# Kernel optimization log

Measured on AMD Instinct MI355X. Metric: run time of the kernel, lower is better.

## Reference

```python
import jax, jax.numpy as jnp
import numpy as np

B, C, R, E, H = 32, 64, 63, 256, 4
D = E // H  # head dim = 64


def setup_inputs() -> dict:
    key = jax.random.key(0)
    ks = jax.random.split(key, 8)
    s = 0.02
    return {
        "x": jax.random.normal(ks[0], (B, C, R, E), jnp.float32),
        "real_cols": jax.random.randint(ks[1], (B,), 0, C),
        "cls_token": jax.random.normal(ks[2], (E,), jnp.float32),
        "w_in": (jax.random.normal(ks[3], (3 * E, E), jnp.float32) * s),
        "b_in": jnp.zeros((3 * E,), jnp.float32),
        "w_out": (jax.random.normal(ks[4], (E, E), jnp.float32) * s),
        "b_out": jnp.zeros((E,), jnp.float32),
        "ln_g": jnp.ones((E,), jnp.float32),
        "ln_b": jnp.zeros((E,), jnp.float32),
        "w1": (jax.random.normal(ks[5], (E, E), jnp.float32) * s),
        "b1": jnp.zeros((E,), jnp.float32),
        "w2": (jax.random.normal(ks[6], (E, E), jnp.float32) * s),
        "b2": jnp.zeros((E,), jnp.float32),
    }


def reference(x, real_cols, cls_token, w_in, b_in, w_out, b_out, ln_g, ln_b, w1, b1, w2, b2):
    # x: (B, C, R, E); one fused batched MHA+LN+FFN over all (B, C) columns.
    Bq, Cq, Rq, Eq = x.shape
    S = Rq + 1
    cls = jnp.broadcast_to(cls_token, (Bq, Cq, 1, Eq))
    seq = jnp.concatenate([cls, x], axis=2)  # (B,C,S,E)

    # torch MultiheadAttention in-projection: x @ W^T + b, packed q|k|v
    qkv = seq @ w_in.T + b_in  # (B,C,S,3E)
    q, k, v = jnp.split(qkv, 3, axis=-1)
    q = q.reshape(Bq, Cq, S, H, D)
    k = k.reshape(Bq, Cq, S, H, D)
    v = v.reshape(Bq, Cq, S, H, D)

    scale = 1.0 / jnp.sqrt(jnp.asarray(D, x.dtype))
    scores = jnp.einsum('bcqhd,bckhd->bchqk', q, k) * scale  # (B,C,H,S,S)
    attn = jax.nn.softmax(scores, axis=-1)
    ctx = jnp.einsum('bchqk,bckhd->bcqhd', attn, v).reshape(Bq, Cq, S, Eq)
    attn_out = ctx @ w_out.T + b_out  # (B,C,S,E)

    # LayerNorm (biased variance, eps=1e-5 as in torch)
    mu = attn_out.mean(axis=-1, keepdims=True)
    var = ((attn_out - mu) ** 2).mean(axis=-1, keepdims=True)
    ln = (attn_out - mu) / jnp.sqrt(var + 1e-5) * ln_g + ln_b

    ffn = jax.nn.relu(ln @ w1.T + b1) @ w2.T + b2
    out = ln + ffn  # (B,C,S,E)

    rep = out[:, :, 0, :]  # rep_mode == 'cls'

    # columns >= real_cols[b] are zero-padded, matching the original loop
    mask = jnp.arange(Cq)[None, :] < real_cols[:, None]
    return jnp.where(mask[..., None], rep, jnp.zeros((), x.dtype))
```

## Files before the change

### kernel.cpp

```cpp
#include <hip/hip_runtime.h>
#include <hip/hip_bf16.h>
#include <cstdint>

typedef unsigned short u16;
typedef uint32_t u32;

#define Bq 32
#define Cq 64
#define Rq 63
#define NB 4

__device__ __forceinline__ float bflo(u32 u){ return __uint_as_float(u << 16); }
__device__ __forceinline__ float bfhi(u32 u){ return __uint_as_float(u & 0xffff0000u); }
__device__ __forceinline__ float bf1(u16 u){ return __uint_as_float(((u32)u) << 16); }
__device__ __forceinline__ u16 tobf(float f){ __hip_bfloat16 h = __float2bfloat16(f); return *(u16*)&h; }

__device__ __forceinline__ bool dtype_is_bf16(const void* ln_g){
    return *(const u32*)ln_g == 0x3F803F80u;
}
__device__ __forceinline__ float ldin(const void* p, int i, bool bf){
    return bf ? bf1(((const u16*)p)[i]) : ((const float*)p)[i];
}


__global__ __launch_bounds__(256) void prep_kernel(
    const void* __restrict__ cls, const void* __restrict__ w_in,
    const void* __restrict__ b_in, const void* __restrict__ w_out,
    const void* __restrict__ w1, const void* __restrict__ w2,
    const void* __restrict__ ln_g_flag,
    float* __restrict__ uf, float* __restrict__ sbf,
    u16* __restrict__ wvT, u16* __restrict__ woT,
    u16* __restrict__ w1T, u16* __restrict__ w2T)
{
    const bool bf = dtype_is_bf16(ln_g_flag);
    const int tid = threadIdx.x;
    const int blk = blockIdx.x;
    __shared__ float q0[256];
    __shared__ float clsf[256];

    if (blk < 256) {
        const int e = blk, j = tid;
        const int dsti = ((j >> 3) * 256 + e) * 8 + (j & 7);
        wvT[dsti] = tobf(ldin(w_in, (512 + e) * 256 + j, bf));
        woT[dsti] = tobf(ldin(w_out, e * 256 + j, bf));
        w1T[dsti] = tobf(ldin(w1,    e * 256 + j, bf));
        w2T[dsti] = tobf(ldin(w2,    e * 256 + j, bf));
        return;
    }

    const int h = blk - 256;
    clsf[tid] = ldin(cls, tid, bf);
    __syncthreads();

    {
        float acc = ldin(b_in, tid, bf);
        #pragma unroll 8
        for (int j = 0; j < 256; ++j)
            acc += ldin(w_in, tid * 256 + j, bf) * clsf[j];
        q0[tid] = acc;
    }
    __syncthreads();

    {
        float ua = 0.f;
        #pragma unroll 8
        for (int d = 0; d < 64; ++d)
            ua += q0[h * 64 + d] * ldin(w_in, (256 + h * 64 + d) * 256 + tid, bf);
        uf[h * 256 + tid] = ua * 0.125f;
    }
    if (tid < 64) {
        float p = q0[h * 64 + tid] * ldin(b_in, 256 + h * 64 + tid, bf);
        #pragma unroll
        for (int off = 32; off; off >>= 1) p += __shfl_xor(p, off);
        if (tid == 0) sbf[h] = p * 0.125f;
    }
}

__global__ __launch_bounds__(256) void attn_kernel(
    const void* __restrict__ x, const int* __restrict__ real_cols,
    const void* __restrict__ cls, const void* __restrict__ ln_g,
    const float* __restrict__ uf, const float* __restrict__ sbf,
    u16* __restrict__ sbuf)
{
    const bool bf = dtype_is_bf16(ln_g);
    const int tid = threadIdx.x;
    const int bc = blockIdx.x;
    const int b = bc >> 6, c = bc & 63;
    if (c >= real_cols[b]) return;

    __shared__ __align__(16) u16   lds_seq[64 * 260];
    __shared__ __align__(16) float lds_u[1024];
    __shared__ __align__(16) float lds_a[256];
    __shared__ float lds_sb[4];

    #pragma unroll
    for (int q = 0; q < 4; ++q) lds_u[q * 256 + tid] = uf[q * 256 + tid];
    if (tid < 4) lds_sb[tid] = sbf[tid];

    if (bf) {
        const u16* xr = (const u16*)x + (size_t)bc * (Rq * 256);
        #pragma unroll
        for (int k = 0; k < 8; ++k) {
            int idx = k * 256 + tid;
            if (idx < 2016) {
                uint4 val = *(const uint4*)(xr + idx * 8);
                int tt = (idx >> 5) + 1;
                int col = (idx & 31) * 8;
                uint2* p = (uint2*)&lds_seq[tt * 260 + col];
                p[0] = make_uint2(val.x, val.y);
                p[1] = make_uint2(val.z, val.w);
            }
        }
        if (tid < 32) {
            uint4 val = *(const uint4*)((const u16*)cls + tid * 8);
            uint2* p = (uint2*)&lds_seq[tid * 8];
            p[0] = make_uint2(val.x, val.y);
            p[1] = make_uint2(val.z, val.w);
        }
    } else {
        const float* xr = (const float*)x + (size_t)bc * (Rq * 256);
        #pragma unroll
        for (int k = 0; k < 16; ++k) {
            int idx = k * 256 + tid;
            if (idx < 4032) {
                float4 v = *(const float4*)(xr + idx * 4);
                int tt = (idx >> 6) + 1;
                int col = (idx & 63) * 4;
                u32 lo = ((u32)tobf(v.y) << 16) | tobf(v.x);
                u32 hi = ((u32)tobf(v.w) << 16) | tobf(v.z);
                *(uint2*)&lds_seq[tt * 260 + col] = make_uint2(lo, hi);
            }
        }
        if (tid < 64) {
            float4 v = *(const float4*)((const float*)cls + tid * 4);
            u32 lo = ((u32)tobf(v.y) << 16) | tobf(v.x);
            u32 hi = ((u32)tobf(v.w) << 16) | tobf(v.z);
            *(uint2*)&lds_seq[tid * 4] = make_uint2(lo, hi);
        }
    }
    __syncthreads();

    const int h = tid >> 6, t = tid & 63;
    float sc = lds_sb[h];
    {
        const u16* srow = &lds_seq[t * 260];
        const float* uh = &lds_u[h * 256];
        #pragma unroll 8
        for (int j = 0; j < 256; j += 4) {
            uint2 pv = *(const uint2*)&srow[j];
            float4 uv = *(const float4*)&uh[j];
            sc += bflo(pv.x) * uv.x + bfhi(pv.x) * uv.y
                + bflo(pv.y) * uv.z + bfhi(pv.y) * uv.w;
        }
    }
    float m = sc;
    #pragma unroll
    for (int off = 32; off; off >>= 1) m = fmaxf(m, __shfl_xor(m, off));
    float ev = __expf(sc - m);
    float sum = ev;
    #pragma unroll
    for (int off = 32; off; off >>= 1) sum += __shfl_xor(sum, off);
    lds_a[t * 4 + h] = ev / sum;
    __syncthreads();

    {
        float s0 = 0.f, s1 = 0.f, s2 = 0.f, s3 = 0.f;
        #pragma unroll 4
        for (int tt = 0; tt < 64; ++tt) {
            float v = bf1(lds_seq[tt * 260 + tid]);
            float4 at = *(const float4*)&lds_a[tt * 4];
            s0 += at.x * v; s1 += at.y * v; s2 += at.z * v; s3 += at.w * v;
        }
        u16* sp = sbuf + (size_t)bc * 1024;
        sp[tid]       = tobf(s0);
        sp[256 + tid] = tobf(s1);
        sp[512 + tid] = tobf(s2);
        sp[768 + tid] = tobf(s3);
    }
}

template<int NBv>
__device__ __forceinline__ void dotN(const u16* __restrict__ wp,
                                     const float* __restrict__ vecs, int vstride,
                                     float* __restrict__ acc)
{
    #pragma unroll 2
    for (int j8 = 0; j8 < 32; ++j8) {
        uint4 w = *(const uint4*)(wp + j8 * 2048);
        float w0 = bflo(w.x), w1_ = bfhi(w.x), w2_ = bflo(w.y), w3 = bfhi(w.y);
        float w4 = bflo(w.z), w5 = bfhi(w.z), w6 = bflo(w.w), w7 = bfhi(w.w);
        #pragma unroll
        for (int i = 0; i < NBv; ++i) {
            const float* v = vecs + i * vstride + j8 * 8;
            float4 a = *(const float4*)v;
            float4 bq = *(const float4*)(v + 4);
            acc[i] += w0 * a.x + w1_ * a.y + w2_ * a.z + w3 * a.w
                    + w4 * bq.x + w5 * bq.y + w6 * bq.z + w7 * bq.w;
        }
    }
}

__global__ __launch_bounds__(256) void ffn_kernel(
    const int* __restrict__ real_cols,
    const void* __restrict__ b_in, const void* __restrict__ b_out,
    const void* __restrict__ ln_g, const void* __restrict__ ln_b,
    const void* __restrict__ b1p, const void* __restrict__ b2p,
    const u16* __restrict__ sbuf,
    const u16* __restrict__ wvT, const u16* __restrict__ woT,
    const u16* __restrict__ w1T, const u16* __restrict__ w2T,
    void* __restrict__ out)
{
    const bool bf = dtype_is_bf16(ln_g);
    const int tid = threadIdx.x;
    const int b = blockIdx.x >> 4;
    const int g = blockIdx.x & 15;
    const int c0 = g * NB;
    const int rc = real_cols[b];
    const int e = tid;

    if (c0 >= rc) {
        #pragma unroll
        for (int i = 0; i < NB; ++i) {
            size_t oi = (((size_t)b << 6) + c0 + i) * 256 + e;
            if (bf) ((u16*)out)[oi] = 0; else ((float*)out)[oi] = 0.f;
        }
        return;
    }

    __shared__ __align__(16) float lds_s[NB * 1024];
    __shared__ __align__(16) float lds_ctx[NB * 256];
    __shared__ __align__(16) float lds_ln[NB * 256];
    __shared__ __align__(16) float lds_h1[NB * 256];
    __shared__ float lds_redA[4 * NB];
    __shared__ float lds_redB[4 * NB];

    #pragma unroll
    for (int i = 0; i < NB; ++i) {
        int c = c0 + i;
        if (c < rc) {
            const u32* sp = (const u32*)(sbuf + ((((size_t)b << 6) + c) << 10));
            u32 a0 = sp[tid], a1 = sp[tid + 256];
            lds_s[i * 1024 + 2 * tid]       = bflo(a0);
            lds_s[i * 1024 + 2 * tid + 1]   = bfhi(a0);
            lds_s[i * 1024 + 512 + 2 * tid]     = bflo(a1);
            lds_s[i * 1024 + 512 + 2 * tid + 1] = bfhi(a1);
        } else {
            lds_s[i * 1024 + 2 * tid] = 0.f;   lds_s[i * 1024 + 2 * tid + 1] = 0.f;
            lds_s[i * 1024 + 512 + 2 * tid] = 0.f; lds_s[i * 1024 + 512 + 2 * tid + 1] = 0.f;
        }
    }
    __syncthreads();

    const int h = tid >> 6;

    {
        float acc[NB];
        float bv = ldin(b_in, 512 + e, bf);
        #pragma unroll
        for (int i = 0; i < NB; ++i) acc[i] = bv;
        dotN<NB>(wvT + e * 8, &lds_s[h * 256], 1024, acc);
        #pragma unroll
        for (int i = 0; i < NB; ++i) lds_ctx[i * 256 + e] = acc[i];
    }
    __syncthreads();

    float ao[NB];
    {
        float bo = ldin(b_out, e, bf);
        #pragma unroll
        for (int i = 0; i < NB; ++i) ao[i] = bo;
        dotN<NB>(woT + e * 8, lds_ctx, 256, ao);
    }

    const int lane = tid & 63, wv = tid >> 6;
    float mu[NB];
    {
        float r[NB];
        #pragma unroll
        for (int i = 0; i < NB; ++i) r[i] = ao[i];
        #pragma unroll
        for (int off = 32; off; off >>= 1) {
            #pragma unroll
            for (int i = 0; i < NB; ++i) r[i] += __shfl_xor(r[i], off);
        }
        if (lane == 0) {
            #pragma unroll
            for (int i = 0; i < NB; ++i) lds_redA[wv * NB + i] = r[i];
        }
    }
    __syncthreads();
    #pragma unroll
    for (int i = 0; i < NB; ++i)
        mu[i] = (lds_redA[i] + lds_redA[NB + i] + lds_redA[2 * NB + i] + lds_redA[3 * NB + i]) * (1.f / 256.f);

    float lnv[NB];
    {
        float r[NB];
        #pragma unroll
        for (int i = 0; i < NB; ++i) { float d = ao[i] - mu[i]; r[i] = d * d; }
        #pragma unroll
        for (int off = 32; off; off >>= 1) {
            #pragma unroll
            for (int i = 0; i < NB; ++i) r[i] += __shfl_xor(r[i], off);
        }
        if (lane == 0) {
            #pragma unroll
            for (int i = 0; i < NB; ++i) lds_redB[wv * NB + i] = r[i];
        }
    }
    __syncthreads();
    {
        float gg = ldin(ln_g, e, bf), bb = ldin(ln_b, e, bf);
        #pragma unroll
        for (int i = 0; i < NB; ++i) {
            float var = (lds_redB[i] + lds_redB[NB + i] + lds_redB[2 * NB + i] + lds_redB[3 * NB + i]) * (1.f / 256.f);
            lnv[i] = (ao[i] - mu[i]) * rsqrtf(var + 1e-5f) * gg + bb;
            lds_ln[i * 256 + e] = lnv[i];
        }
    }
    __syncthreads();

    {
        float h1[NB];
        float bv = ldin(b1p, e, bf);
        #pragma unroll
        for (int i = 0; i < NB; ++i) h1[i] = bv;
        dotN<NB>(w1T + e * 8, lds_ln, 256, h1);
        #pragma unroll
        for (int i = 0; i < NB; ++i) lds_h1[i * 256 + e] = fmaxf(h1[i], 0.f);
    }
    __syncthreads();

    {
        float o[NB];
        float bv = ldin(b2p, e, bf);
        #pragma unroll
        for (int i = 0; i < NB; ++i) o[i] = lnv[i] + bv;
        dotN<NB>(w2T + e * 8, lds_h1, 256, o);
        #pragma unroll
        for (int i = 0; i < NB; ++i) {
            int c = c0 + i;
            float val = (c < rc) ? o[i] : 0.f;
            size_t oi = (((size_t)b << 6) + c) * 256 + e;
            if (bf) ((u16*)out)[oi] = tobf(val); else ((float*)out)[oi] = val;
        }
    }
}

extern "C" void kernel_launch(void* const* d_in, const int* in_sizes, int n_in,
                              void* d_out, int out_size, void* d_ws, size_t ws_size,
                              hipStream_t stream) {
    const void* x     = d_in[0];
    const int* rcols  = (const int*)d_in[1];
    const void* cls   = d_in[2];
    const void* w_in  = d_in[3];
    const void* b_in  = d_in[4];
    const void* w_out = d_in[5];
    const void* b_out = d_in[6];
    const void* ln_g  = d_in[7];
    const void* ln_b  = d_in[8];
    const void* w1    = d_in[9];
    const void* b1    = d_in[10];
    const void* w2    = d_in[11];
    const void* b2    = d_in[12];

    char* ws = (char*)d_ws;
    float* uf  = (float*)(ws);
    float* sbf = (float*)(ws + 4096);
    u16* wvT = (u16*)(ws + 4608);
    u16* woT = (u16*)(ws + 4608 + 131072);
    u16* w1T = (u16*)(ws + 4608 + 2 * 131072);
    u16* w2T = (u16*)(ws + 4608 + 3 * 131072);
    u16* sbuf = (u16*)(ws + 528896);

    prep_kernel<<<260, 256, 0, stream>>>(cls, w_in, b_in, w_out, w1, w2, ln_g,
                                         uf, sbf, wvT, woT, w1T, w2T);
    attn_kernel<<<Bq * Cq, 256, 0, stream>>>(x, rcols, cls, ln_g, uf, sbf, sbuf);
    ffn_kernel<<<Bq * (Cq / NB), 256, 0, stream>>>(rcols, b_in, b_out, ln_g, ln_b,
                                                   b1, b2, sbuf,
                                                   wvT, woT, w1T, w2T, d_out);
}
```

Measured before the change: 276.6 us.

## Split FFN reductions across two thread halves and move weight transpose into attention launch

The weight transpose/bf16 conversion blocks move from the prep kernel into extra blocks of the attention launch. This shortens the serial prep step so it no longer delays attention. The FFN kernel now uses 512 threads, with each half computing half of the K-dimension dot products and combining partials through LDS, giving more parallelism per block at the cost of extra syncs. The attention weighted-sum stage uses 128 threads, each handling two adjacent elements with packed 32-bit loads and stores.

Result: slower. 293.4 us (+6.1%).

```diff
diff --git a/kernel.cpp b/kernel.cpp
--- a/kernel.cpp
+++ b/kernel.cpp
@@ -23,32 +23,17 @@
 }
 
 
-__global__ __launch_bounds__(256) void prep_kernel(
+__global__ __launch_bounds__(256) void prep_u_kernel(
     const void* __restrict__ cls, const void* __restrict__ w_in,
-    const void* __restrict__ b_in, const void* __restrict__ w_out,
-    const void* __restrict__ w1, const void* __restrict__ w2,
-    const void* __restrict__ ln_g_flag,
-    float* __restrict__ uf, float* __restrict__ sbf,
-    u16* __restrict__ wvT, u16* __restrict__ woT,
-    u16* __restrict__ w1T, u16* __restrict__ w2T)
+    const void* __restrict__ b_in, const void* __restrict__ ln_g_flag,
+    float* __restrict__ uf, float* __restrict__ sbf)
 {
     const bool bf = dtype_is_bf16(ln_g_flag);
     const int tid = threadIdx.x;
-    const int blk = blockIdx.x;
+    const int h = blockIdx.x;
     __shared__ float q0[256];
     __shared__ float clsf[256];
 
-    if (blk < 256) {
-        const int e = blk, j = tid;
-        const int dsti = ((j >> 3) * 256 + e) * 8 + (j & 7);
-        wvT[dsti] = tobf(ldin(w_in, (512 + e) * 256 + j, bf));
-        woT[dsti] = tobf(ldin(w_out, e * 256 + j, bf));
-        w1T[dsti] = tobf(ldin(w1,    e * 256 + j, bf));
-        w2T[dsti] = tobf(ldin(w2,    e * 256 + j, bf));
-        return;
-    }
-
-    const int h = blk - 256;
     clsf[tid] = ldin(cls, tid, bf);
     __syncthreads();
 
@@ -79,12 +64,27 @@
 __global__ __launch_bounds__(256) void attn_kernel(
     const void* __restrict__ x, const int* __restrict__ real_cols,
     const void* __restrict__ cls, const void* __restrict__ ln_g,
+    const void* __restrict__ w_in, const void* __restrict__ w_out,
+    const void* __restrict__ w1, const void* __restrict__ w2,
     const float* __restrict__ uf, const float* __restrict__ sbf,
+    u16* __restrict__ wvT, u16* __restrict__ woT,
+    u16* __restrict__ w1T, u16* __restrict__ w2T,
     u16* __restrict__ sbuf)
 {
     const bool bf = dtype_is_bf16(ln_g);
     const int tid = threadIdx.x;
     const int bc = blockIdx.x;
+
+    if (bc >= 2048) {
+        const int e2 = bc - 2048, j = tid;
+        const int dsti = ((j >> 3) * 256 + e2) * 8 + (j & 7);
+        wvT[dsti] = tobf(ldin(w_in, (512 + e2) * 256 + j, bf));
+        woT[dsti] = tobf(ldin(w_out, e2 * 256 + j, bf));
+        w1T[dsti] = tobf(ldin(w1,    e2 * 256 + j, bf));
+        w2T[dsti] = tobf(ldin(w2,    e2 * 256 + j, bf));
+        return;
+    }
+
     const int b = bc >> 6, c = bc & 63;
     if (c >= real_cols[b]) return;
 
@@ -163,29 +163,33 @@
     lds_a[t * 4 + h] = ev / sum;
     __syncthreads();
 
-    {
-        float s0 = 0.f, s1 = 0.f, s2 = 0.f, s3 = 0.f;
+    if (tid < 128) {
+        const int j2 = tid;
+        float s00 = 0.f, s01 = 0.f, s02 = 0.f, s03 = 0.f;
+        float s10 = 0.f, s11 = 0.f, s12 = 0.f, s13 = 0.f;
         #pragma unroll 4
         for (int tt = 0; tt < 64; ++tt) {
-            float v = bf1(lds_seq[tt * 260 + tid]);
+            u32 pv = *(const u32*)&lds_seq[tt * 260 + 2 * j2];
+            float vlo = bflo(pv), vhi = bfhi(pv);
             float4 at = *(const float4*)&lds_a[tt * 4];
-            s0 += at.x * v; s1 += at.y * v; s2 += at.z * v; s3 += at.w * v;
-        }
-        u16* sp = sbuf + (size_t)bc * 1024;
-        sp[tid]       = tobf(s0);
-        sp[256 + tid] = tobf(s1);
-        sp[512 + tid] = tobf(s2);
-        sp[768 + tid] = tobf(s3);
+            s00 += at.x * vlo; s01 += at.y * vlo; s02 += at.z * vlo; s03 += at.w * vlo;
+            s10 += at.x * vhi; s11 += at.y * vhi; s12 += at.z * vhi; s13 += at.w * vhi;
+        }
+        u32* sp32 = (u32*)(sbuf + (size_t)bc * 1024);
+        sp32[        j2] = (u32)tobf(s00) | ((u32)tobf(s10) << 16);
+        sp32[128 +   j2] = (u32)tobf(s01) | ((u32)tobf(s11) << 16);
+        sp32[256 +   j2] = (u32)tobf(s02) | ((u32)tobf(s12) << 16);
+        sp32[384 +   j2] = (u32)tobf(s03) | ((u32)tobf(s13) << 16);
     }
 }
 
 template<int NBv>
-__device__ __forceinline__ void dotN(const u16* __restrict__ wp,
-                                     const float* __restrict__ vecs, int vstride,
-                                     float* __restrict__ acc)
+__device__ __forceinline__ void dot_half(const u16* __restrict__ wp, int j0,
+                                         const float* __restrict__ vecs, int vstride,
+                                         float* __restrict__ acc)
 {
-    #pragma unroll 2
-    for (int j8 = 0; j8 < 32; ++j8) {
+    #pragma unroll 4
+    for (int j8 = j0; j8 < j0 + 16; ++j8) {
         uint4 w = *(const uint4*)(wp + j8 * 2048);
         float w0 = bflo(w.x), w1_ = bfhi(w.x), w2_ = bflo(w.y), w3 = bfhi(w.y);
         float w4 = bflo(w.z), w5 = bfhi(w.z), w6 = bflo(w.w), w7 = bfhi(w.w);
@@ -200,7 +204,7 @@
     }
 }
 
-__global__ __launch_bounds__(256) void ffn_kernel(
+__global__ __launch_bounds__(512) void ffn_kernel(
     const int* __restrict__ real_cols,
     const void* __restrict__ b_in, const void* __restrict__ b_out,
     const void* __restrict__ ln_g, const void* __restrict__ ln_b,
@@ -212,68 +216,77 @@
 {
     const bool bf = dtype_is_bf16(ln_g);
     const int tid = threadIdx.x;
+    const int e = tid & 255;
+    const int half = tid >> 8;
+    const int wave = tid >> 6;
     const int b = blockIdx.x >> 4;
     const int g = blockIdx.x & 15;
     const int c0 = g * NB;
     const int rc = real_cols[b];
-    const int e = tid;
 
     if (c0 >= rc) {
         #pragma unroll
-        for (int i = 0; i < NB; ++i) {
-            size_t oi = (((size_t)b << 6) + c0 + i) * 256 + e;
+        for (int k = 0; k < 2; ++k) {
+            int flat = k * 512 + tid;
+            int c = c0 + (flat >> 8), e2 = flat & 255;
+            size_t oi = (((size_t)b << 6) + c) * 256 + e2;
             if (bf) ((u16*)out)[oi] = 0; else ((float*)out)[oi] = 0.f;
         }
         return;
     }
 
     __shared__ __align__(16) float lds_s[NB * 1024];
-    __shared__ __align__(16) float lds_ctx[NB * 256];
-    __shared__ __align__(16) float lds_ln[NB * 256];
-    __shared__ __align__(16) float lds_h1[NB * 256];
-    __shared__ float lds_redA[4 * NB];
-    __shared__ float lds_redB[4 * NB];
-
-    #pragma unroll
-    for (int i = 0; i < NB; ++i) {
-        int c = c0 + i;
-        if (c < rc) {
-            const u32* sp = (const u32*)(sbuf + ((((size_t)b << 6) + c) << 10));
-            u32 a0 = sp[tid], a1 = sp[tid + 256];
-            lds_s[i * 1024 + 2 * tid]       = bflo(a0);
-            lds_s[i * 1024 + 2 * tid + 1]   = bfhi(a0);
-            lds_s[i * 1024 + 512 + 2 * tid]     = bflo(a1);
-            lds_s[i * 1024 + 512 + 2 * tid + 1] = bfhi(a1);
-        } else {
-            lds_s[i * 1024 + 2 * tid] = 0.f;   lds_s[i * 1024 + 2 * tid + 1] = 0.f;
-            lds_s[i * 1024 + 512 + 2 * tid] = 0.f; lds_s[i * 1024 + 512 + 2 * tid + 1] = 0.f;
-        }
-    }
-    __syncthreads();
-
-    const int h = tid >> 6;
-
-    {
-        float acc[NB];
+    __shared__ __align__(16) float lds_p[2 * NB * 256];
+    __shared__ __align__(16) float lds_vec[NB * 256];
+    __shared__ float lds_redA[32], lds_redB[32];
+
+    #pragma unroll
+    for (int k = 0; k < 4; ++k) {
+        int d = k * 512 + tid;
+        int col = d >> 9, pos = d & 511;
+        int c = c0 + col;
+        u32 dw = 0;
+        if (c < rc) dw = ((const u32*)sbuf)[((((size_t)b << 6) + c) << 9) + pos];
+        lds_s[col * 1024 + 2 * pos]     = bflo(dw);
+        lds_s[col * 1024 + 2 * pos + 1] = bfhi(dw);
+    }
+    __syncthreads();
+
+    const int j0 = half * 16;
+    const int hE = e >> 6;
+    float acc[NB];
+
+    #pragma unroll
+    for (int i = 0; i < NB; ++i) acc[i] = 0.f;
+    dot_half<NB>(wvT + e * 8, j0, &lds_s[hE * 256], 1024, acc);
+    #pragma unroll
+    for (int i = 0; i < NB; ++i) lds_p[half * 1024 + i * 256 + e] = acc[i];
+    __syncthreads();
+    {
         float bv = ldin(b_in, 512 + e, bf);
-        #pragma unroll
-        for (int i = 0; i < NB; ++i) acc[i] = bv;
-        dotN<NB>(wvT + e * 8, &lds_s[h * 256], 1024, acc);
-        #pragma unroll
-        for (int i = 0; i < NB; ++i) lds_ctx[i * 256 + e] = acc[i];
-    }
+        if (!half) {
+            #pragma unroll
+            for (int i = 0; i < NB; ++i)
+                lds_vec[i * 256 + e] = lds_p[i * 256 + e] + lds_p[1024 + i * 256 + e] + bv;
+        }
+    }
+    __syncthreads();
+
+    #pragma unroll
+    for (int i = 0; i < NB; ++i) acc[i] = 0.f;
+    dot_half<NB>(woT + e * 8, j0, lds_vec, 256, acc);
+    #pragma unroll
+    for (int i = 0; i < NB; ++i) lds_p[half * 1024 + i * 256 + e] = acc[i];
     __syncthreads();
 
     float ao[NB];
     {
         float bo = ldin(b_out, e, bf);
         #pragma unroll
-        for (int i = 0; i < NB; ++i) ao[i] = bo;
-        dotN<NB>(woT + e * 8, lds_ctx, 256, ao);
-    }
-
-    const int lane = tid & 63, wv = tid >> 6;
-    float mu[NB];
+        for (int i = 0; i < NB; ++i)
+            ao[i] = lds_p[i * 256 + e] + lds_p[1024 + i * 256 + e] + bo;
+    }
+
     {
         float r[NB];
         #pragma unroll
@@ -283,17 +296,16 @@
             #pragma unroll
             for (int i = 0; i < NB; ++i) r[i] += __shfl_xor(r[i], off);
         }
-        if (lane == 0) {
-            #pragma unroll
-            for (int i = 0; i < NB; ++i) lds_redA[wv * NB + i] = r[i];
-        }
-    }
-    __syncthreads();
+        if ((tid & 63) == 0) {
+            #pragma unroll
+            for (int i = 0; i < NB; ++i) lds_redA[wave * NB + i] = r[i];
+        }
+    }
+    __syncthreads();
+    float mu[NB], lnv[NB];
     #pragma unroll
     for (int i = 0; i < NB; ++i)
         mu[i] = (lds_redA[i] + lds_redA[NB + i] + lds_redA[2 * NB + i] + lds_redA[3 * NB + i]) * (1.f / 256.f);
-
-    float lnv[NB];
     {
         float r[NB];
         #pragma unroll
@@ -303,9 +315,9 @@
             #pragma unroll
             for (int i = 0; i < NB; ++i) r[i] += __shfl_xor(r[i], off);
         }
-        if (lane == 0) {
-            #pragma unroll
-            for (int i = 0; i < NB; ++i) lds_redB[wv * NB + i] = r[i];
+        if ((tid & 63) == 0) {
+            #pragma unroll
+            for (int i = 0; i < NB; ++i) lds_redB[wave * NB + i] = r[i];
         }
     }
     __syncthreads();
@@ -315,32 +327,43 @@
         for (int i = 0; i < NB; ++i) {
             float var = (lds_redB[i] + lds_redB[NB + i] + lds_redB[2 * NB + i] + lds_redB[3 * NB + i]) * (1.f / 256.f);
             lnv[i] = (ao[i] - mu[i]) * rsqrtf(var + 1e-5f) * gg + bb;
-            lds_ln[i * 256 + e] = lnv[i];
-        }
-    }
-    __syncthreads();
-
-    {
-        float h1[NB];
+        }
+        if (!half) {
+            #pragma unroll
+            for (int i = 0; i < NB; ++i) lds_vec[i * 256 + e] = lnv[i];
+        }
+    }
+    __syncthreads();
+
+    #pragma unroll
+    for (int i = 0; i < NB; ++i) acc[i] = 0.f;
+    dot_half<NB>(w1T + e * 8, j0, lds_vec, 256, acc);
+    #pragma unroll
+    for (int i = 0; i < NB; ++i) lds_p[half * 1024 + i * 256 + e] = acc[i];
+    __syncthreads();
+    {
         float bv = ldin(b1p, e, bf);
-        #pragma unroll
-        for (int i = 0; i < NB; ++i) h1[i] = bv;
-        dotN<NB>(w1T + e * 8, lds_ln, 256, h1);
-        #pragma unroll
-        for (int i = 0; i < NB; ++i) lds_h1[i * 256 + e] = fmaxf(h1[i], 0.f);
-    }
-    __syncthreads();
-
-    {
-        float o[NB];
+        if (!half) {
+            #pragma unroll
+            for (int i = 0; i < NB; ++i)
+                lds_vec[i * 256 + e] = fmaxf(lds_p[i * 256 + e] + lds_p[1024 + i * 256 + e] + bv, 0.f);
+        }
+    }
+    __syncthreads();
+
+    #pragma unroll
+    for (int i = 0; i < NB; ++i) acc[i] = 0.f;
+    dot_half<NB>(w2T + e * 8, j0, lds_vec, 256, acc);
+    #pragma unroll
+    for (int i = 0; i < NB; ++i) lds_p[half * 1024 + i * 256 + e] = acc[i];
+    __syncthreads();
+    if (!half) {
         float bv = ldin(b2p, e, bf);
-        #pragma unroll
-        for (int i = 0; i < NB; ++i) o[i] = lnv[i] + bv;
-        dotN<NB>(w2T + e * 8, lds_h1, 256, o);
         #pragma unroll
         for (int i = 0; i < NB; ++i) {
             int c = c0 + i;
-            float val = (c < rc) ? o[i] : 0.f;
+            float o = lnv[i] + bv + lds_p[i * 256 + e] + lds_p[1024 + i * 256 + e];
+            float val = (c < rc) ? o : 0.f;
             size_t oi = (((size_t)b << 6) + c) * 256 + e;
             if (bf) ((u16*)out)[oi] = tobf(val); else ((float*)out)[oi] = val;
         }
@@ -373,10 +396,11 @@
     u16* w2T = (u16*)(ws + 4608 + 3 * 131072);
     u16* sbuf = (u16*)(ws + 528896);
 
-    prep_kernel<<<260, 256, 0, stream>>>(cls, w_in, b_in, w_out, w1, w2, ln_g,
-                                         uf, sbf, wvT, woT, w1T, w2T);
-    attn_kernel<<<Bq * Cq, 256, 0, stream>>>(x, rcols, cls, ln_g, uf, sbf, sbuf);
-    ffn_kernel<<<Bq * (Cq / NB), 256, 0, stream>>>(rcols, b_in, b_out, ln_g, ln_b,
-                                                   b1, b2, sbuf,
-                                                   wvT, woT, w1T, w2T, d_out);
-}
+    prep_u_kernel<<<4, 256, 0, stream>>>(cls, w_in, b_in, ln_g, uf, sbf);
+    attn_kernel<<<2048 + 256, 256, 0, stream>>>(x, rcols, cls, ln_g,
+                                                w_in, w_out, w1, w2,
+                                                uf, sbf, wvT, woT, w1T, w2T, sbuf);
+    ffn_kernel<<<Bq * 16, 512, 0, stream>>>(rcols, b_in, b_out, ln_g, ln_b,
+                                            b1, b2, sbuf,
+                                            wvT, woT, w1T, w2T, d_out);
+}
```
